# Kernel optimization log

Hardware: AMD Instinct MI355X
Metric: run time of the kernel (lower is better)

The kernel has to match this reference:

```python
import jax, jax.numpy as jnp
import numpy as np

# Config matching init_kwargs / input shapes
DIM = 96        # dim == C
NH = 6          # num_heads
KS = 7          # kernel_size (local window)
GW = 4          # group_width for the grouped conv in Hadamard-attn branch
B, D, H, W = 2, 8, 96, 96
HD = DIM // NH          # head dim (dim_qk == dim_v == dim)
SCALE = HD ** -0.5      # qk_scale default: head_dim**-0.5
PAD = KS // 2
EPS = 1e-5


def setup_inputs() -> dict:
    key = jax.random.key(0)
    ks = jax.random.split(key, 10)
    s = 0.02
    return {
        "x": jax.random.normal(ks[0], (B, DIM, D, H, W), jnp.float32),
        # pre-norm LayerNorm params
        "ln_g": jnp.ones((DIM,), jnp.float32),
        "ln_b": jnp.zeros((DIM,), jnp.float32),
        # q,k projection (fused 1x1): out = 2*dim_qk
        "w_qk": s * jax.random.normal(ks[1], (2 * DIM, DIM), jnp.float32),
        "b_qk": jnp.zeros((2 * DIM,), jnp.float32),
        # v projection (1x1)
        "w_v": s * jax.random.normal(ks[2], (DIM, DIM), jnp.float32),
        "b_v": jnp.zeros((DIM,), jnp.float32),
        # Hadamard-attention branch: grouped KSxKS conv (groups = DIM//GW)
        "w_a1": s * jax.random.normal(ks[3], (DIM, GW, KS, KS), jnp.float32),
        "b_a1": jnp.zeros((DIM,), jnp.float32),
        # 1x1 conv producing per-head local attention logits (NH * KS^2 channels)
        "w_a2": s * jax.random.normal(ks[4], (NH * KS * KS, DIM), jnp.float32),
        "b_a2": jnp.zeros((NH * KS * KS,), jnp.float32),
        # ghost head (lam=1, gamma=1): attn = h_attn * ghost_mul + ghost_add
        "g_mul": 1.0 + s * jax.random.normal(ks[5], (NH * KS * KS,), jnp.float32),
        "g_add": s * jax.random.normal(ks[6], (NH * KS * KS,), jnp.float32),
        # output projection (1x1)
        "w_p": s * jax.random.normal(ks[7], (DIM, DIM), jnp.float32),
        "b_p": jnp.zeros((DIM,), jnp.float32),
    }


def _elsa_block(x, ln_g, ln_b, w_qk, b_qk, w_v, b_v, w_a1, b_a1, w_a2, b_a2,
                g_mul, g_add, w_p, b_p):
    """x: (Bp, H, W, C) channel-last frames. Pre-norm residual ELSA attention."""
    Bp, Hh, Ww, C = x.shape
    # LayerNorm over channels
    mu = jnp.mean(x, axis=-1, keepdims=True)
    var = jnp.mean(jnp.square(x - mu), axis=-1, keepdims=True)
    xn = (x - mu) * jax.lax.rsqrt(var + EPS) * ln_g + ln_b

    # 1x1 q,k,v projections (channel-last matmuls)
    qk = xn @ w_qk.T + b_qk                      # (Bp,H,W,2C)
    q, k = jnp.split(qk, 2, axis=-1)
    v = xn @ w_v.T + b_v                         # (Bp,H,W,C)

    # Hadamard product -> attention logits via grouped conv + GELU + 1x1
    h = jnp.transpose(q * k * SCALE, (0, 3, 1, 2))   # (Bp,C,H,W) NCHW
    a = jax.lax.conv_general_dilated(
        h, w_a1, window_strides=(1, 1), padding='SAME',
        feature_group_count=C // GW) + b_a1[None, :, None, None]
    a = jax.nn.gelu(a, approximate=False)
    a = jnp.einsum('bchw,oc->bohw', a, w_a2) + b_a2[None, :, None, None]

    # ghost head (lam=1, gamma=1): elementwise scale + static bias per (head, tap)
    attn = a * g_mul[None, :, None, None] + g_add[None, :, None, None]
    attn = attn.reshape(Bp, NH, KS * KS, Hh, Ww)     # (Bp,nh,k^2,H,W)

    # local window aggregation (unfold-free: 49 shifted fused multiply-adds)
    vr = jnp.transpose(v, (0, 3, 1, 2)).reshape(Bp, NH, HD, Hh, Ww)
    vp = jnp.pad(vr, ((0, 0), (0, 0), (0, 0), (PAD, PAD), (PAD, PAD)))
    out = jnp.zeros_like(vr)
    for i in range(KS):
        for j in range(KS):
            out = out + attn[:, :, i * KS + j, None] * vp[:, :, :, i:i + Hh, j:j + Ww]

    out = jnp.transpose(out.reshape(Bp, C, Hh, Ww), (0, 2, 3, 1))  # (Bp,H,W,C)
    y = out @ w_p.T + b_p
    return x + y


def reference(x, ln_g, ln_b, w_qk, b_qk, w_v, b_v, w_a1, b_a1, w_a2, b_a2,
              g_mul, g_add, w_p, b_p):
    b, c, d, hh, ww = x.shape
    # 'b c s h w -> (b s) h w c'
    xf = jnp.transpose(x, (0, 2, 3, 4, 1)).reshape(b * d, hh, ww, c)
    yf = _elsa_block(xf, ln_g, ln_b, w_qk, b_qk, w_v, b_v, w_a1, b_a1,
                     w_a2, b_a2, g_mul, g_add, w_p, b_p)
    # '(b s) h w c -> b c s h w'
    return jnp.transpose(yf.reshape(b, d, hh, ww, c), (0, 4, 1, 2, 3))
```

## Files before the change

### kernel.cpp

```cpp
#include <hip/hip_runtime.h>
#include <hip/hip_bf16.h>


typedef unsigned short u16;
typedef short bf16x8 __attribute__((ext_vector_type(8)));
typedef float floatx4 __attribute__((ext_vector_type(4)));
typedef unsigned short ushort8 __attribute__((ext_vector_type(8)));
typedef unsigned int uint4v __attribute__((ext_vector_type(4)));
typedef unsigned int uint2v __attribute__((ext_vector_type(2)));
typedef _Float16 f16x2 __attribute__((ext_vector_type(2)));

#define PIX      9216
#define SCALE_QK 0.25f

__device__ __forceinline__ float lo2f(unsigned int u) {
  union { unsigned int i; float f; } z; z.i = u << 16; return z.f;
}
__device__ __forceinline__ float hi2f(unsigned int u) {
  union { unsigned int i; float f; } z; z.i = u & 0xFFFF0000u; return z.f;
}
__device__ __forceinline__ u16 f2b(float f) {
  union { float f; unsigned int i; } z; z.f = f;
  unsigned int r = z.i + 0x7fffu + ((z.i >> 16) & 1u);
  return (u16)(r >> 16);
}
__device__ __forceinline__ u16 f2h(float f) {
  _Float16 h = (_Float16)f;
  union { _Float16 h; u16 u; } z; z.h = h; return z.u;
}
__device__ __forceinline__ f16x2 upk(unsigned int u) {
  union { unsigned int u; f16x2 h; } z; z.u = u; return z.h;
}
__device__ __forceinline__ f16x2 pkfma(unsigned int w, unsigned int x, f16x2 c) {
#if __has_builtin(__builtin_elementwise_fma)
  return __builtin_elementwise_fma(upk(w), upk(x), c);
#else
  return upk(w) * upk(x) + c;
#endif
}

__global__ void k_prep(const float* __restrict__ w_qk, const float* __restrict__ b_qk,
                       const float* __restrict__ w_v,  const float* __restrict__ b_v,
                       const float* __restrict__ w_a1,
                       const float* __restrict__ w_a2, const float* __restrict__ b_a2,
                       const float* __restrict__ g_mul,const float* __restrict__ g_add,
                       const float* __restrict__ w_p,  const float* __restrict__ b_p,
                       u16* __restrict__ W2, float* __restrict__ bias2,
                       u16* __restrict__ WA2, float* __restrict__ biasA2,
                       u16* __restrict__ WP, float* __restrict__ biasP,
                       unsigned int* __restrict__ WCV) {
  int i = blockIdx.x * 256 + threadIdx.x;
  if (i < 30720) {
    int r = i / 96, ci = i % 96;
    float val = 0.f;
    if (r < 192) { int src = (r & 1) ? (96 + (r >> 1)) : (r >> 1); val = w_qk[src * 96 + ci]; }
    else if (r < 288) val = w_v[(r - 192) * 96 + ci];
    W2[i] = f2b(val);
  } else if (i < 31040) {
    int r = i - 30720; float bv = 0.f;
    if (r < 192) { int src = (r & 1) ? (96 + (r >> 1)) : (r >> 1); bv = b_qk[src]; }
    else if (r < 288) bv = b_v[r - 192];
    bias2[r] = bv;
  } else if (i < 61760) {
    int j = i - 31040; int r = j / 96, ci = j % 96;
    float wv = 0.f;
    if (r < 294) wv = w_a2[r * 96 + ci] * g_mul[r];
    WA2[j] = f2b(wv);
  } else if (i < 62080) {
    int r = i - 61760; float bv = 0.f;
    if (r < 294) bv = b_a2[r] * g_mul[r] + g_add[r];
    biasA2[r] = bv;
  } else if (i < 74368) {
    int j = i - 62080; int r = j / 96;
    WP[j] = (r < 96) ? f2b(w_p[j]) : (u16)0;
  } else if (i < 74496) {
    int r = i - 74368;
    biasP[r] = (r < 96) ? b_p[r] : 0.f;
  } else if (i < 93312) {
    int j = i - 74496;
    int kx = j % 7, co = (j / 7) & 3, ky = (j / 28) % 7, ch = (j / 196) & 3, g = j / 784;
    float w = w_a1[(g * 4 + co) * 196 + ch * 49 + ky * 7 + kx];
    unsigned int hw = f2h(w);
    WCV[j] = hw | (hw << 16);
  }
}

__global__ __launch_bounds__(256) void k_ln(const float* __restrict__ x,
                                            const float* __restrict__ lg,
                                            const float* __restrict__ lb,
                                            u16* __restrict__ xn) {
  int idx = blockIdx.x * 256 + threadIdx.x;
  int f = idx / PIX, p = idx % PIX;
  int b = f >> 3, d = f & 7;
  size_t base = ((size_t)(b * 768 + d)) * PIX + p;
  float s = 0.f, ss = 0.f;
  for (int c = 0; c < 96; ++c) {
    float v = x[base + (size_t)c * 73728];
    s += v; ss += v * v;
  }
  float mu = s * (1.f / 96.f);
  float var = ss * (1.f / 96.f) - mu * mu;
  float rs = rsqrtf(var + 1e-5f);
  size_t ob = (size_t)idx * 96;
  for (int c0 = 0; c0 < 96; c0 += 8) {
    ushort8 pack;
    for (int u = 0; u < 8; ++u) {
      int c = c0 + u;
      float v = x[base + (size_t)c * 73728];
      pack[u] = f2b((v - mu) * rs * lg[c] + lb[c]);
    }
    *(ushort8*)&xn[ob + c0] = pack;
  }
}

template <int MODE>
__global__ __launch_bounds__(256) void k_gemm(const u16* __restrict__ X,
                                              const u16* __restrict__ W,
                                              const float* __restrict__ bias,
                                              u16* __restrict__ out0,
                                              u16* __restrict__ out1,
                                              float* __restrict__ outF,
                                              const float* __restrict__ resid,
                                              int fArg) {
  __shared__ u16 lw[64 * 104];
  __shared__ u16 lx[64 * 104];
  const int tid = threadIdx.x;
  const int fc = blockIdx.z;
  const int f = (MODE == 1) ? (fArg + fc) : fc;
  const int p0 = blockIdx.x * 64;
  const int cot = blockIdx.y;

  if constexpr (MODE == 0) {
    for (int ch = tid; ch < 768; ch += 256) {
      int r = ch / 12, s2 = ch % 12;
      *(uint4v*)&lw[r * 104 + s2 * 8] = *(const uint4v*)&W[(size_t)(cot * 64 + r) * 96 + s2 * 8];
      *(uint4v*)&lx[r * 104 + s2 * 8] = *(const uint4v*)&X[((size_t)(f * PIX + p0 + r)) * 96 + s2 * 8];
    }
  } else {
    for (int ch = tid; ch < 768; ch += 256) {
      int r = ch / 12, s2 = ch % 12;
      *(uint4v*)&lw[r * 104 + s2 * 8] = *(const uint4v*)&W[(size_t)(cot * 64 + r) * 96 + s2 * 8];
    }
    for (int idx = tid; idx < 768; idx += 256) {
      int s2 = idx >> 6, r = idx & 63;
      const u16* src0 = &X[((size_t)(f * 24 + 2 * s2) * PIX + p0 + r) * 4];
      const u16* src1 = &X[((size_t)(f * 24 + 2 * s2 + 1) * PIX + p0 + r) * 4];
      *(uint2v*)&lx[r * 104 + s2 * 8]     = *(const uint2v*)src0;
      *(uint2v*)&lx[r * 104 + s2 * 8 + 4] = *(const uint2v*)src1;
    }
  }
  __syncthreads();

  const int lane = tid & 63, wv = tid >> 6;
  const int cw = (wv >> 1) * 32, pw = (wv & 1) * 32;
  const int m = lane & 15, quad = lane >> 4;

  floatx4 acc[2][2] = {};
  for (int ks = 0; ks < 3; ++ks) {
    int ko = ks * 32 + quad * 8;
    bf16x8 a0 = *(const bf16x8*)&lw[(cw + m) * 104 + ko];
    bf16x8 a1 = *(const bf16x8*)&lw[(cw + 16 + m) * 104 + ko];
    bf16x8 b0 = *(const bf16x8*)&lx[(pw + m) * 104 + ko];
    bf16x8 b1 = *(const bf16x8*)&lx[(pw + 16 + m) * 104 + ko];
    acc[0][0] = __builtin_amdgcn_mfma_f32_16x16x32_bf16(a0, b0, acc[0][0], 0, 0, 0);
    acc[0][1] = __builtin_amdgcn_mfma_f32_16x16x32_bf16(a0, b1, acc[0][1], 0, 0, 0);
    acc[1][0] = __builtin_amdgcn_mfma_f32_16x16x32_bf16(a1, b0, acc[1][0], 0, 0, 0);
    acc[1][1] = __builtin_amdgcn_mfma_f32_16x16x32_bf16(a1, b1, acc[1][1], 0, 0, 0);
  }

  for (int mt = 0; mt < 2; ++mt)
    for (int nt = 0; nt < 2; ++nt) {
      int R = cot * 64 + cw + mt * 16 + quad * 4;
      int pc = p0 + pw + nt * 16 + m;
      floatx4 v4 = acc[mt][nt];
      if (MODE == 0) {
        if (cot < 3) {
          float q0 = v4[0] + bias[R + 0], k0 = v4[1] + bias[R + 1];
          float q1 = v4[2] + bias[R + 2], k1 = v4[3] + bias[R + 3];
          int hc = R >> 1;
          out0[((size_t)f * 96 + hc) * PIX + pc]     = f2h(q0 * k0 * SCALE_QK);
          out0[((size_t)f * 96 + hc + 1) * PIX + pc] = f2h(q1 * k1 * SCALE_QK);
        } else {
          for (int r = 0; r < 4; ++r) {
            int vr = R + r - 192;
            if (vr < 96) out1[((size_t)f * 96 + vr) * PIX + pc] = f2b(v4[r] + bias[R + r]);
          }
        }
      } else if (MODE == 1) {
        for (int r = 0; r < 4; ++r) {
          int o = R + r;
          if (o < 294) out0[((size_t)fc * 294 + o) * PIX + pc] = f2b(v4[r] + bias[o]);
        }
      } else {
        int b = f >> 3, d = f & 7;
        for (int r = 0; r < 4; ++r) {
          int o = R + r;
          if (o < 96) {
            size_t gi = ((size_t)(b * 96 + o) * 8 + d) * PIX + pc;
            outF[gi] = resid[gi] + v4[r] + bias[o];
          }
        }
      }
    }
}

__global__ __launch_bounds__(256, 4) void k_conv(const u16* __restrict__ h,
                                                 const unsigned int* __restrict__ wcv,
                                                 const float* __restrict__ b_a1,
                                                 u16* __restrict__ a_t) {
  __shared__ u16 li[4 * 22 * 104];
  const int g = blockIdx.x, ty = blockIdx.y, f = blockIdx.z;
  const int tid = threadIdx.x;
  const int gb = g * 4, y0 = ty * 16;
  for (int idx = tid; idx < 4576; idx += 256) {
    int row = idx / 52;
    int jd  = idx - row * 52;
    int ch  = row / 22;
    int rr  = row - ch * 22;
    int ay  = y0 - 3 + rr;
    unsigned int val = 0;
    if (jd >= 2 && jd <= 49 && ay >= 0 && ay < 96)
      val = *(const unsigned int*)&h[((size_t)f * 96 + gb + ch) * PIX + ay * 96 + (2 * jd - 4)];
    *(unsigned int*)&li[row * 104 + 2 * jd] = val;
  }
  __syncthreads();

  const int y = tid >> 4;
  const int x0 = (tid & 15) * 6;
  f16x2 pacc[4][3];
  #pragma unroll
  for (int co = 0; co < 4; ++co)
    #pragma unroll
    for (int p = 0; p < 3; ++p) pacc[co][p] = upk(0u);

  for (int ch = 0; ch < 4; ++ch) {
    const unsigned int* wch = &wcv[784 * g + 196 * ch];
    for (int ky = 0; ky < 7; ++ky) {
      const unsigned int* lsrc =
          (const unsigned int*)&li[(ch * 22 + (y + ky)) * 104 + x0];
      unsigned int D0 = lsrc[0], D1 = lsrc[1], D2 = lsrc[2], D3 = lsrc[3];
      unsigned int D4 = lsrc[4], D5 = lsrc[5], D6 = lsrc[6];
      unsigned int S0 = __builtin_amdgcn_alignbit(D1, D0, 16);
      unsigned int S1 = __builtin_amdgcn_alignbit(D2, D1, 16);
      unsigned int S2 = __builtin_amdgcn_alignbit(D3, D2, 16);
      unsigned int S3 = __builtin_amdgcn_alignbit(D4, D3, 16);
      unsigned int S4 = __builtin_amdgcn_alignbit(D5, D4, 16);
      unsigned int S5 = __builtin_amdgcn_alignbit(D6, D5, 16);
      const unsigned int* wb = wch + 28 * ky;
      #pragma unroll
      for (int co = 0; co < 4; ++co) {
        unsigned int w0 = wb[co * 7 + 0], w1 = wb[co * 7 + 1];
        unsigned int w2 = wb[co * 7 + 2], w3 = wb[co * 7 + 3];
        unsigned int w4 = wb[co * 7 + 4], w5 = wb[co * 7 + 5];
        unsigned int w6 = wb[co * 7 + 6];
        f16x2 a;
        a = pacc[co][0];
        a = pkfma(w0, S0, a); a = pkfma(w1, D1, a); a = pkfma(w2, S1, a);
        a = pkfma(w3, D2, a); a = pkfma(w4, S2, a); a = pkfma(w5, D3, a);
        a = pkfma(w6, S3, a); pacc[co][0] = a;
        a = pacc[co][1];
        a = pkfma(w0, S1, a); a = pkfma(w1, D2, a); a = pkfma(w2, S2, a);
        a = pkfma(w3, D3, a); a = pkfma(w4, S3, a); a = pkfma(w5, D4, a);
        a = pkfma(w6, S4, a); pacc[co][1] = a;
        a = pacc[co][2];
        a = pkfma(w0, S2, a); a = pkfma(w1, D3, a); a = pkfma(w2, S3, a);
        a = pkfma(w3, D4, a); a = pkfma(w4, S4, a); a = pkfma(w5, D5, a);
        a = pkfma(w6, S5, a); pacc[co][2] = a;
      }
    }
  }

  size_t obase = ((size_t)(f * 24 + g) * PIX + (size_t)(y0 + y) * 96 + x0) * 4;
  float bv0 = b_a1[gb + 0], bv1 = b_a1[gb + 1], bv2 = b_a1[gb + 2], bv3 = b_a1[gb + 3];
  #pragma unroll
  for (int p = 0; p < 3; ++p) {
    ushort8 r8;
    #pragma unroll
    for (int co = 0; co < 4; ++co) {
      float bv = (co == 0) ? bv0 : (co == 1) ? bv1 : (co == 2) ? bv2 : bv3;
      f16x2 v = pacc[co][p];
      float a0 = (float)v[0] + bv, a1 = (float)v[1] + bv;
      r8[co]     = f2b(0.5f * a0 * (1.f + erff(a0 * 0.70710678118f)));
      r8[co + 4] = f2b(0.5f * a1 * (1.f + erff(a1 * 0.70710678118f)));
    }
    *(ushort8*)&a_t[obase + p * 8] = r8;
  }
}

__global__ __launch_bounds__(256, 4) void k_aggr(const u16* __restrict__ attn_c,
                                                 const u16* __restrict__ v,
                                                 u16* __restrict__ out_t,
                                                 int fbase) {
  __shared__ u16 lv[4 * 22 * 104];
  const int wgid = blockIdx.x + 24 * (blockIdx.y + 6 * blockIdx.z);
  const int xcd = wgid & 7;
  const int member = (wgid >> 3) & 3;
  const int slot = wgid >> 5;
  const int gidx = slot * 8 + xcd;
  const int cqh = gidx % 6;
  const int ty = (gidx / 6) % 6;
  const int fc = gidx / 36;
  const int cq = cqh * 4 + member;
  const int f = fbase + fc;
  const int tid = threadIdx.x;
  const int c0 = cq * 4, y0 = ty * 16;
  const int head = c0 >> 4;
  for (int idx = tid; idx < 4 * 22 * 104; idx += 256) {
    int col = idx % 104;
    int rr = (idx / 104) % 22;
    int ch = idx / (104 * 22);
    int ax = col - 3, ay = y0 - 3 + rr;
    u16 val = 0;
    if (ax >= 0 && ax < 96 && ay >= 0 && ay < 96)
      val = v[((size_t)f * 96 + c0 + ch) * PIX + ay * 96 + ax];
    lv[idx] = val;
  }
  __syncthreads();

  const int y = tid >> 4;
  const int x0 = (tid & 15) * 6;
  float acc[4][6] = {};
  const int prow = (y0 + y) * 96 + x0;

  for (int i = 0; i < 7; ++i) {
    float vrow[4][12];
    #pragma unroll
    for (int ch = 0; ch < 4; ++ch) {
      const unsigned int* lsrc = (const unsigned int*)&lv[(ch * 22 + (y + i)) * 104 + x0];
      #pragma unroll
      for (int t = 0; t < 6; ++t) {
        unsigned int u = lsrc[t];
        vrow[ch][2 * t]     = lo2f(u);
        vrow[ch][2 * t + 1] = hi2f(u);
      }
    }
    #pragma unroll
    for (int j = 0; j < 7; ++j) {
      const unsigned int* asrc = (const unsigned int*)
          &attn_c[((size_t)fc * 294 + head * 49 + i * 7 + j) * PIX + prow];
      unsigned int u0 = asrc[0], u1 = asrc[1], u2 = asrc[2];
      float av[6] = {lo2f(u0), hi2f(u0), lo2f(u1), hi2f(u1), lo2f(u2), hi2f(u2)};
      #pragma unroll
      for (int o = 0; o < 6; ++o)
        #pragma unroll
        for (int ch = 0; ch < 4; ++ch)
          acc[ch][o] += av[o] * vrow[ch][o + j];
    }
  }

  size_t obase = ((size_t)(f * 24 + cq) * PIX + prow) * 4;
  #pragma unroll
  for (int o = 0; o < 6; o += 2) {
    ushort8 r8;
    #pragma unroll
    for (int ch = 0; ch < 4; ++ch) {
      r8[ch]     = f2b(acc[ch][o]);
      r8[ch + 4] = f2b(acc[ch][o + 1]);
    }
    *(ushort8*)&out_t[obase + o * 4] = r8;
  }
}

extern "C" void kernel_launch(void* const* d_in, const int* in_sizes, int n_in,
                              void* d_out, int out_size, void* d_ws, size_t ws_size,
                              hipStream_t stream) {
  const float* x    = (const float*)d_in[0];
  const float* ln_g = (const float*)d_in[1];
  const float* ln_b = (const float*)d_in[2];
  const float* w_qk = (const float*)d_in[3];
  const float* b_qk = (const float*)d_in[4];
  const float* w_v  = (const float*)d_in[5];
  const float* b_v  = (const float*)d_in[6];
  const float* w_a1 = (const float*)d_in[7];
  const float* b_a1 = (const float*)d_in[8];
  const float* w_a2 = (const float*)d_in[9];
  const float* b_a2 = (const float*)d_in[10];
  const float* g_mul= (const float*)d_in[11];
  const float* g_add= (const float*)d_in[12];
  const float* w_p  = (const float*)d_in[13];
  const float* b_p  = (const float*)d_in[14];

  char* ws = (char*)d_ws;
  u16*   W2    = (u16*)(ws + 0);
  float* bias2 = (float*)(ws + 61440);
  u16*   WA2   = (u16*)(ws + 62720);
  float* biasA2= (float*)(ws + 124160);
  u16*   WP    = (u16*)(ws + 125440);
  float* biasP = (float*)(ws + 150016);
  unsigned int* WCV = (unsigned int*)(ws + 150528);
  u16*   xn_t  = (u16*)(ws + 225792);
  u16*   hbuf  = (u16*)(ws + 28537344);
  u16*   vbuf  = (u16*)(ws + 56848896);
  u16*   attnc = (u16*)(ws + 85160448);

  k_prep<<<365, 256, 0, stream>>>(w_qk, b_qk, w_v, b_v, w_a1, w_a2, b_a2, g_mul, g_add,
                                  w_p, b_p, W2, bias2, WA2, biasA2, WP, biasP, WCV);
  k_ln<<<576, 256, 0, stream>>>(x, ln_g, ln_b, xn_t);
  k_gemm<0><<<dim3(144, 5, 16), 256, 0, stream>>>(xn_t, W2, bias2, hbuf, vbuf,
                                                  nullptr, nullptr, 0);
  k_conv<<<dim3(24, 6, 16), 256, 0, stream>>>(hbuf, WCV, b_a1, xn_t );
  for (int c = 0; c < 2; ++c) {
    k_gemm<1><<<dim3(144, 5, 8), 256, 0, stream>>>(xn_t , WA2, biasA2,
                                                   attnc, nullptr, nullptr, nullptr, c * 8);
    k_aggr<<<dim3(24, 6, 8), 256, 0, stream>>>(attnc, vbuf, hbuf , c * 8);
  }
  k_gemm<2><<<dim3(144, 2, 16), 256, 0, stream>>>(hbuf , WP, biasP,
                                                  nullptr, nullptr, (float*)d_out, x, 0);
}
```

Measured before the change: 395.4 us.

## Fuse LayerNorm into QKV GEMM and loop output-channel tiles per block

Removes the standalone LayerNorm kernel. The first GEMM now reads the channel-first fp32 input directly, computes per-pixel mean and variance with four threads per pixel and shuffle reductions, and writes normalized bf16 into shared memory. All GEMM modes now loop over every output-channel tile inside one block instead of launching a grid dimension per tile, so the activation tile is loaded once and reused. This saves the xn round trip through global memory and repeated X loads. In exchange the grid becomes smaller, adds extra barriers per tile, and runs the weight loads serially within each block.

Measured after the change: 378.7 us. 4.2% less time.

```diff
diff --git a/kernel.cpp b/kernel.cpp
--- a/kernel.cpp
+++ b/kernel.cpp
@@ -85,34 +85,6 @@
   }
 }
 
-__global__ __launch_bounds__(256) void k_ln(const float* __restrict__ x,
-                                            const float* __restrict__ lg,
-                                            const float* __restrict__ lb,
-                                            u16* __restrict__ xn) {
-  int idx = blockIdx.x * 256 + threadIdx.x;
-  int f = idx / PIX, p = idx % PIX;
-  int b = f >> 3, d = f & 7;
-  size_t base = ((size_t)(b * 768 + d)) * PIX + p;
-  float s = 0.f, ss = 0.f;
-  for (int c = 0; c < 96; ++c) {
-    float v = x[base + (size_t)c * 73728];
-    s += v; ss += v * v;
-  }
-  float mu = s * (1.f / 96.f);
-  float var = ss * (1.f / 96.f) - mu * mu;
-  float rs = rsqrtf(var + 1e-5f);
-  size_t ob = (size_t)idx * 96;
-  for (int c0 = 0; c0 < 96; c0 += 8) {
-    ushort8 pack;
-    for (int u = 0; u < 8; ++u) {
-      int c = c0 + u;
-      float v = x[base + (size_t)c * 73728];
-      pack[u] = f2b((v - mu) * rs * lg[c] + lb[c]);
-    }
-    *(ushort8*)&xn[ob + c0] = pack;
-  }
-}
-
 template <int MODE>
 __global__ __launch_bounds__(256) void k_gemm(const u16* __restrict__ X,
                                               const u16* __restrict__ W,
@@ -121,26 +93,42 @@
                                               u16* __restrict__ out1,
                                               float* __restrict__ outF,
                                               const float* __restrict__ resid,
+                                              const float* __restrict__ lg,
+                                              const float* __restrict__ lb,
                                               int fArg) {
+  constexpr int NC = (MODE == 2) ? 2 : 5;
   __shared__ u16 lw[64 * 104];
   __shared__ u16 lx[64 * 104];
   const int tid = threadIdx.x;
-  const int fc = blockIdx.z;
+  const int fc = blockIdx.y;
   const int f = (MODE == 1) ? (fArg + fc) : fc;
   const int p0 = blockIdx.x * 64;
-  const int cot = blockIdx.y;
 
   if constexpr (MODE == 0) {
-    for (int ch = tid; ch < 768; ch += 256) {
-      int r = ch / 12, s2 = ch % 12;
-      *(uint4v*)&lw[r * 104 + s2 * 8] = *(const uint4v*)&W[(size_t)(cot * 64 + r) * 96 + s2 * 8];
-      *(uint4v*)&lx[r * 104 + s2 * 8] = *(const uint4v*)&X[((size_t)(f * PIX + p0 + r)) * 96 + s2 * 8];
+    const int pix = tid >> 2, sub = tid & 3;
+    const int b = f >> 3, d = f & 7;
+    const size_t xbase = ((size_t)(b * 768 + d)) * PIX + p0 + pix;
+    float xv[24];
+    #pragma unroll
+    for (int k = 0; k < 24; ++k)
+      xv[k] = resid[xbase + (size_t)(sub * 24 + k) * 73728];
+    float s = 0.f, ss = 0.f;
+    #pragma unroll
+    for (int k = 0; k < 24; ++k) { s += xv[k]; ss += xv[k] * xv[k]; }
+    s += __shfl_xor(s, 1);  ss += __shfl_xor(ss, 1);
+    s += __shfl_xor(s, 2);  ss += __shfl_xor(ss, 2);
+    float mu = s * (1.f / 96.f);
+    float var = ss * (1.f / 96.f) - mu * mu;
+    float rs = rsqrtf(var + 1e-5f);
+    unsigned int* dst = (unsigned int*)&lx[pix * 104 + sub * 24];
+    #pragma unroll
+    for (int k = 0; k < 12; ++k) {
+      int c = sub * 24 + 2 * k;
+      u16 lo = f2b((xv[2 * k]     - mu) * rs * lg[c]     + lb[c]);
+      u16 hi = f2b((xv[2 * k + 1] - mu) * rs * lg[c + 1] + lb[c + 1]);
+      dst[k] = (unsigned int)lo | ((unsigned int)hi << 16);
     }
   } else {
-    for (int ch = tid; ch < 768; ch += 256) {
-      int r = ch / 12, s2 = ch % 12;
-      *(uint4v*)&lw[r * 104 + s2 * 8] = *(const uint4v*)&W[(size_t)(cot * 64 + r) * 96 + s2 * 8];
-    }
     for (int idx = tid; idx < 768; idx += 256) {
       int s2 = idx >> 6, r = idx & 63;
       const u16* src0 = &X[((size_t)(f * 24 + 2 * s2) * PIX + p0 + r) * 4];
@@ -155,53 +143,63 @@
   const int cw = (wv >> 1) * 32, pw = (wv & 1) * 32;
   const int m = lane & 15, quad = lane >> 4;
 
-  floatx4 acc[2][2] = {};
-  for (int ks = 0; ks < 3; ++ks) {
-    int ko = ks * 32 + quad * 8;
-    bf16x8 a0 = *(const bf16x8*)&lw[(cw + m) * 104 + ko];
-    bf16x8 a1 = *(const bf16x8*)&lw[(cw + 16 + m) * 104 + ko];
-    bf16x8 b0 = *(const bf16x8*)&lx[(pw + m) * 104 + ko];
-    bf16x8 b1 = *(const bf16x8*)&lx[(pw + 16 + m) * 104 + ko];
-    acc[0][0] = __builtin_amdgcn_mfma_f32_16x16x32_bf16(a0, b0, acc[0][0], 0, 0, 0);
-    acc[0][1] = __builtin_amdgcn_mfma_f32_16x16x32_bf16(a0, b1, acc[0][1], 0, 0, 0);
-    acc[1][0] = __builtin_amdgcn_mfma_f32_16x16x32_bf16(a1, b0, acc[1][0], 0, 0, 0);
-    acc[1][1] = __builtin_amdgcn_mfma_f32_16x16x32_bf16(a1, b1, acc[1][1], 0, 0, 0);
-  }
-
-  for (int mt = 0; mt < 2; ++mt)
-    for (int nt = 0; nt < 2; ++nt) {
-      int R = cot * 64 + cw + mt * 16 + quad * 4;
-      int pc = p0 + pw + nt * 16 + m;
-      floatx4 v4 = acc[mt][nt];
-      if (MODE == 0) {
-        if (cot < 3) {
-          float q0 = v4[0] + bias[R + 0], k0 = v4[1] + bias[R + 1];
-          float q1 = v4[2] + bias[R + 2], k1 = v4[3] + bias[R + 3];
-          int hc = R >> 1;
-          out0[((size_t)f * 96 + hc) * PIX + pc]     = f2h(q0 * k0 * SCALE_QK);
-          out0[((size_t)f * 96 + hc + 1) * PIX + pc] = f2h(q1 * k1 * SCALE_QK);
+  for (int cot = 0; cot < NC; ++cot) {
+    for (int ch = tid; ch < 768; ch += 256) {
+      int r = ch / 12, s2 = ch % 12;
+      *(uint4v*)&lw[r * 104 + s2 * 8] =
+          *(const uint4v*)&W[(size_t)(cot * 64 + r) * 96 + s2 * 8];
+    }
+    __syncthreads();
+
+    floatx4 acc[2][2] = {};
+    for (int ks = 0; ks < 3; ++ks) {
+      int ko = ks * 32 + quad * 8;
+      bf16x8 a0 = *(const bf16x8*)&lw[(cw + m) * 104 + ko];
+      bf16x8 a1 = *(const bf16x8*)&lw[(cw + 16 + m) * 104 + ko];
+      bf16x8 b0 = *(const bf16x8*)&lx[(pw + m) * 104 + ko];
+      bf16x8 b1 = *(const bf16x8*)&lx[(pw + 16 + m) * 104 + ko];
+      acc[0][0] = __builtin_amdgcn_mfma_f32_16x16x32_bf16(a0, b0, acc[0][0], 0, 0, 0);
+      acc[0][1] = __builtin_amdgcn_mfma_f32_16x16x32_bf16(a0, b1, acc[0][1], 0, 0, 0);
+      acc[1][0] = __builtin_amdgcn_mfma_f32_16x16x32_bf16(a1, b0, acc[1][0], 0, 0, 0);
+      acc[1][1] = __builtin_amdgcn_mfma_f32_16x16x32_bf16(a1, b1, acc[1][1], 0, 0, 0);
+    }
+
+    for (int mt = 0; mt < 2; ++mt)
+      for (int nt = 0; nt < 2; ++nt) {
+        int R = cot * 64 + cw + mt * 16 + quad * 4;
+        int pc = p0 + pw + nt * 16 + m;
+        floatx4 v4 = acc[mt][nt];
+        if (MODE == 0) {
+          if (cot < 3) {
+            float q0 = v4[0] + bias[R + 0], k0 = v4[1] + bias[R + 1];
+            float q1 = v4[2] + bias[R + 2], k1 = v4[3] + bias[R + 3];
+            int hc = R >> 1;
+            out0[((size_t)f * 96 + hc) * PIX + pc]     = f2h(q0 * k0 * SCALE_QK);
+            out0[((size_t)f * 96 + hc + 1) * PIX + pc] = f2h(q1 * k1 * SCALE_QK);
+          } else {
+            for (int r = 0; r < 4; ++r) {
+              int vr = R + r - 192;
+              if (vr < 96) out1[((size_t)f * 96 + vr) * PIX + pc] = f2b(v4[r] + bias[R + r]);
+            }
+          }
+        } else if (MODE == 1) {
+          for (int r = 0; r < 4; ++r) {
+            int o = R + r;
+            if (o < 294) out0[((size_t)fc * 294 + o) * PIX + pc] = f2b(v4[r] + bias[o]);
+          }
         } else {
+          int b = f >> 3, dd = f & 7;
           for (int r = 0; r < 4; ++r) {
-            int vr = R + r - 192;
-            if (vr < 96) out1[((size_t)f * 96 + vr) * PIX + pc] = f2b(v4[r] + bias[R + r]);
-          }
-        }
-      } else if (MODE == 1) {
-        for (int r = 0; r < 4; ++r) {
-          int o = R + r;
-          if (o < 294) out0[((size_t)fc * 294 + o) * PIX + pc] = f2b(v4[r] + bias[o]);
-        }
-      } else {
-        int b = f >> 3, d = f & 7;
-        for (int r = 0; r < 4; ++r) {
-          int o = R + r;
-          if (o < 96) {
-            size_t gi = ((size_t)(b * 96 + o) * 8 + d) * PIX + pc;
-            outF[gi] = resid[gi] + v4[r] + bias[o];
+            int o = R + r;
+            if (o < 96) {
+              size_t gi = ((size_t)(b * 96 + o) * 8 + dd) * PIX + pc;
+              outF[gi] = resid[gi] + v4[r] + bias[o];
+            }
           }
         }
       }
-    }
+    __syncthreads();
+  }
 }
 
 __global__ __launch_bounds__(256, 4) void k_conv(const u16* __restrict__ h,
@@ -388,22 +386,23 @@
   u16*   WP    = (u16*)(ws + 125440);
   float* biasP = (float*)(ws + 150016);
   unsigned int* WCV = (unsigned int*)(ws + 150528);
-  u16*   xn_t  = (u16*)(ws + 225792);
+  u16*   a_t   = (u16*)(ws + 225792);
   u16*   hbuf  = (u16*)(ws + 28537344);
   u16*   vbuf  = (u16*)(ws + 56848896);
   u16*   attnc = (u16*)(ws + 85160448);
 
   k_prep<<<365, 256, 0, stream>>>(w_qk, b_qk, w_v, b_v, w_a1, w_a2, b_a2, g_mul, g_add,
                                   w_p, b_p, W2, bias2, WA2, biasA2, WP, biasP, WCV);
-  k_ln<<<576, 256, 0, stream>>>(x, ln_g, ln_b, xn_t);
-  k_gemm<0><<<dim3(144, 5, 16), 256, 0, stream>>>(xn_t, W2, bias2, hbuf, vbuf,
-                                                  nullptr, nullptr, 0);
-  k_conv<<<dim3(24, 6, 16), 256, 0, stream>>>(hbuf, WCV, b_a1, xn_t );
+  k_gemm<0><<<dim3(144, 16), 256, 0, stream>>>(nullptr, W2, bias2, hbuf, vbuf,
+                                               nullptr, x, ln_g, ln_b, 0);
+  k_conv<<<dim3(24, 6, 16), 256, 0, stream>>>(hbuf, WCV, b_a1, a_t);
   for (int c = 0; c < 2; ++c) {
-    k_gemm<1><<<dim3(144, 5, 8), 256, 0, stream>>>(xn_t , WA2, biasA2,
-                                                   attnc, nullptr, nullptr, nullptr, c * 8);
+    k_gemm<1><<<dim3(144, 8), 256, 0, stream>>>(a_t, WA2, biasA2,
+                                                attnc, nullptr, nullptr, nullptr,
+                                                nullptr, nullptr, c * 8);
     k_aggr<<<dim3(24, 6, 8), 256, 0, stream>>>(attnc, vbuf, hbuf , c * 8);
   }
-  k_gemm<2><<<dim3(144, 2, 16), 256, 0, stream>>>(hbuf , WP, biasP,
-                                                  nullptr, nullptr, (float*)d_out, x, 0);
-}
+  k_gemm<2><<<dim3(144, 16), 256, 0, stream>>>(hbuf , WP, biasP,
+                                               nullptr, nullptr, (float*)d_out, x,
+                                               nullptr, nullptr, 0);
+}
```
